# Kernel optimization log

Measured on AMD Instinct MI355X. Metric: run time of the kernel, lower is better.

## Reference

```python
import jax, jax.numpy as jnp
import numpy as np

B, T, D = 4, 4096, 1024
H, HD, K = 16, 64, 32
TAU, THRESHOLD, PULSE_BASE, N_STEPS = 0.1, 0.5, 4.0, 5


def setup_inputs() -> dict:
    key = jax.random.key(0)
    ks = jax.random.split(key, 8)
    s = 0.02
    return {
        "x": jax.random.normal(ks[0], (B, T, D), jnp.float32),
        "spectral_basis": jax.random.normal(ks[1], (B, T, K), jnp.float32) / np.sqrt(T),
        "W_qkv": jax.random.normal(ks[2], (3 * D, D), jnp.float32) * s,
        "W_out": jax.random.normal(ks[3], (D, D), jnp.float32) * s,
        "a": jnp.float32(0.7),
        "b": jnp.float32(0.8),
        "W1": jax.random.normal(ks[4], (HD // 2, HD), jnp.float32) * s,
        "b1": jnp.zeros((HD // 2,), jnp.float32),
        "W2": jax.random.normal(ks[5], (1, HD // 2), jnp.float32) * s,
        "b2": jnp.zeros((1,), jnp.float32),
        "spectral_filter": jnp.full((H, 32), 0.5, jnp.float32),
    }


def soliton_dynamics(stimulus, a, b):
    # stimulus: (B, H, K, HD); FitzHugh-Nagumo style 5-step Euler integration
    dt = 1.0 / N_STEPS
    v = jnp.zeros_like(stimulus)
    w = jnp.zeros_like(stimulus)
    stim_scale = jnp.clip(jnp.max(jnp.abs(stimulus), axis=-1, keepdims=True), 1e-06, None)
    stim_n = stimulus / stim_scale
    I = jnp.where(jnp.abs(stimulus) > THRESHOLD, stim_n, stim_n * 0.1)
    for _ in range(N_STEPS):
        dv = v - v ** 3 / 3 - w + I
        dw = (v + a - b * w) / TAU
        v = jnp.clip(v + dt * dv, -3.0, 3.0)
        w = jnp.clip(w + dt * dw, -3.0, 3.0)
    return v * stim_scale, v


def reference(x, spectral_basis, W_qkv, W_out, a, b, W1, b1, W2, b2, spectral_filter):
    Bx, Tx, Dx = x.shape
    k = spectral_basis.shape[-1]
    qkv = x @ W_qkv.T                                   # (B,T,3D)
    qkv = qkv.reshape(Bx, Tx, 3, H, HD).transpose(2, 0, 3, 1, 4)
    q, kk, v = qkv[0], qkv[1], qkv[2]                   # (B,H,T,HD)

    qm = q.mean(axis=2)                                 # (B,H,HD)
    h1 = jax.nn.silu(qm @ W1.T + b1)
    pulse_widths = PULSE_BASE + jax.nn.softplus(h1 @ W2.T + b2)[..., 0]  # (B,H)

    q_spec = jnp.einsum('bhtd,btk->bhkd', q, spectral_basis)
    k_spec = jnp.einsum('bhtd,btk->bhkd', kk, spectral_basis)
    attn_spec = jnp.einsum('bhkd,bhkd->bhk', q_spec, k_spec) / np.sqrt(HD)
    filt = jax.nn.sigmoid(spectral_filter[:, :k])       # (H,k)
    attn_spec = attn_spec * filt[None]

    stim = jnp.broadcast_to(attn_spec[..., None], (Bx, H, k, HD))
    response, state = soliton_dynamics(stim, a, b)
    response = response.mean(axis=-1)                   # (B,H,k)

    v_spec = jnp.einsum('bhtd,btk->bhkd', v, spectral_basis)
    out_spec = response[..., None] * v_spec             # (B,H,k,HD)
    out = jnp.einsum('bhkd,btk->bhtd', out_spec, spectral_basis)
    out = out.transpose(0, 2, 1, 3).reshape(Bx, Tx, Dx)
    out = out @ W_out.T
    return out, pulse_widths, response
```

## Files before the change

### kernel.cpp

```cpp
#include <hip/hip_runtime.h>

#define B_ 4
#define T_ 4096
#define D_ 1024
#define H_ 16
#define K_ 32


__device__ __forceinline__ void fma4(float4& a, float s, const float4& v){
  a.x = fmaf(s, v.x, a.x); a.y = fmaf(s, v.y, a.y);
  a.z = fmaf(s, v.z, a.z); a.w = fmaf(s, v.w, a.w);
}

__global__ __launch_bounds__(256) void reduce_g(
    const float4* __restrict__ src, float4* __restrict__ dst,
    const int n4, const int zper, const int stride4)
{
  const int g = blockIdx.y;
  int i = blockIdx.x * 256 + threadIdx.x;
  if (i >= n4) return;
  float s0 = 0.f, s1 = 0.f, s2 = 0.f, s3 = 0.f;
  const float4* p = src + (size_t)g * zper * stride4 + i;
  #pragma unroll 8
  for (int zz = 0; zz < zper; ++zz){
    float4 v = p[(size_t)zz * stride4];
    s0 += v.x; s1 += v.y; s2 += v.z; s3 += v.w;
  }
  float4 o; o.x = s0; o.y = s1; o.z = s2; o.w = s3;
  dst[(size_t)g * stride4 + i] = o;
}

__global__ __launch_bounds__(256) void reduce_zp(
    const float4* __restrict__ src, float4* __restrict__ dst,
    const int n4, const int z, const int stride4, const int total4)
{
  int i = blockIdx.x * 256 + threadIdx.x;
  if (i >= total4) return;
  if (i >= n4){
    float4 zv; zv.x = 0.f; zv.y = 0.f; zv.z = 0.f; zv.w = 0.f;
    dst[i] = zv; return;
  }
  float s0 = 0.f, s1 = 0.f, s2 = 0.f, s3 = 0.f;
  const float4* p = src + i;
  #pragma unroll 8
  for (int zz = 0; zz < z; ++zz){
    float4 v = p[(size_t)zz * stride4];
    s0 += v.x; s1 += v.y; s2 += v.z; s3 += v.w;
  }
  float4 o; o.x = s0; o.y = s1; o.z = s2; o.w = s3;
  dst[i] = o;
}

__global__ __launch_bounds__(256) void reduce_z(
    const float4* __restrict__ src, float4* __restrict__ dst,
    const int n4, const int z, const int stride4)
{
  int i = blockIdx.x * 256 + threadIdx.x;
  if (i >= n4) return;
  float s0 = 0.f, s1 = 0.f, s2 = 0.f, s3 = 0.f;
  const float4* p = src + i;
  #pragma unroll 8
  for (int zz = 0; zz < z; ++zz){
    float4 v = p[(size_t)zz * stride4];
    s0 += v.x; s1 += v.y; s2 += v.z; s3 += v.w;
  }
  float4 o; o.x = s0; o.y = s1; o.z = s2; o.w = s3;
  dst[i] = o;
}

__global__ __launch_bounds__(256) void k1_spectral_p(
    const float* __restrict__ x, const float* __restrict__ sb,
    float* __restrict__ XP)
{
  const int ct = blockIdx.x;
  const int b  = blockIdx.y;
  const int zz = blockIdx.z;
  const int t0 = zz * 64;
  const int cs = threadIdx.x & 63;
  const int kg = threadIdx.x >> 6;
  __shared__ __align__(16) float4 xt[4096];
  __shared__ __align__(16) float sbs[64][36];
  #pragma unroll
  for (int i = 0; i < 8; i++){
    int idx = threadIdx.x + i * 256;
    int t = idx >> 5, kk = idx & 31;
    sbs[t][kk] = sb[(size_t)(b * T_ + t0 + t) * K_ + kk];
  }
  const float4* xg = (const float4*)(x + (size_t)(b * T_ + t0) * D_ + ct * 256);
  float4 rv[16];
  #pragma unroll
  for (int j = 0; j < 16; j++){
    int idx = threadIdx.x + j * 256;
    int t = idx >> 6, cq = idx & 63;
    rv[j] = xg[(size_t)t * 256 + cq];
  }
  #pragma unroll
  for (int j = 0; j < 16; j++) xt[threadIdx.x + j * 256] = rv[j];
  __syncthreads();

  float4 acc[8];
  #pragma unroll
  for (int k = 0; k < 8; k++){ acc[k].x = 0.f; acc[k].y = 0.f;
                               acc[k].z = 0.f; acc[k].w = 0.f; }
  float4 am; am.x = 0.f; am.y = 0.f; am.z = 0.f; am.w = 0.f;
  #pragma unroll 4
  for (int t = 0; t < 64; ++t){
    float4 xv = xt[t * 64 + cs];
    if (kg == 0){ am.x += xv.x; am.y += xv.y; am.z += xv.z; am.w += xv.w; }
    const float4* srow = (const float4*)&sbs[t][kg * 8];
    float4 s0 = srow[0], s1 = srow[1];
    fma4(acc[0], s0.x, xv); fma4(acc[1], s0.y, xv);
    fma4(acc[2], s0.z, xv); fma4(acc[3], s0.w, xv);
    fma4(acc[4], s1.x, xv); fma4(acc[5], s1.y, xv);
    fma4(acc[6], s1.z, xv); fma4(acc[7], s1.w, xv);
  }
  const int c = ct * 256 + cs * 4;
  float* o = XP + (size_t)zz * 135168 + (size_t)(b * K_ + kg * 8) * D_ + c;
  #pragma unroll
  for (int k = 0; k < 8; k++) *(float4*)(o + (size_t)k * D_) = acc[k];
  if (kg == 0)
    *(float4*)(XP + (size_t)zz * 135168 + 131072 + b * D_ + c) = am;
}

__global__ __launch_bounds__(256) void gemm_aw_p(
    const float* __restrict__ A, const float* __restrict__ W,
    float* __restrict__ Cp, const int N, const int cPerSplit, const int MN)
{
  __shared__ __align__(16) float As[32][68];
  __shared__ __align__(16) float Ws[32][68];
  const int nt = blockIdx.x, mt = blockIdx.y;
  const int cbase = blockIdx.z * cPerSplit;
  const int tx = threadIdx.x & 15, ty = threadIdx.x >> 4;
  const int sc = threadIdx.x & 31, sr = threadIdx.x >> 5;
  float acc[4][4];
  #pragma unroll
  for (int i = 0; i < 4; i++)
    #pragma unroll
    for (int j = 0; j < 4; j++) acc[i][j] = 0.f;

  float ra[8], rw[8];
  const float* Ap = A + (size_t)(mt * 64 + sr) * 1024 + cbase + sc;
  const float* Wp = W + (size_t)(nt * 64 + sr) * 1024 + cbase + sc;
  #pragma unroll
  for (int i = 0; i < 8; i++){ ra[i] = Ap[(size_t)(i * 8) * 1024];
                               rw[i] = Wp[(size_t)(i * 8) * 1024]; }
  #pragma unroll
  for (int i = 0; i < 8; i++){ As[sc][sr + i * 8] = ra[i];
                               Ws[sc][sr + i * 8] = rw[i]; }
  __syncthreads();

  for (int cc = 32; cc < cPerSplit; cc += 32){
    #pragma unroll
    for (int i = 0; i < 8; i++){ ra[i] = Ap[(size_t)(i * 8) * 1024 + cc];
                                 rw[i] = Wp[(size_t)(i * 8) * 1024 + cc]; }
    #pragma unroll 4
    for (int c = 0; c < 32; ++c){
      const float4 a4 = *(const float4*)&As[c][ty * 4];
      const float4 w4 = *(const float4*)&Ws[c][tx * 4];
      acc[0][0] = fmaf(a4.x, w4.x, acc[0][0]);
      acc[0][1] = fmaf(a4.x, w4.y, acc[0][1]);
      acc[0][2] = fmaf(a4.x, w4.z, acc[0][2]);
      acc[0][3] = fmaf(a4.x, w4.w, acc[0][3]);
      acc[1][0] = fmaf(a4.y, w4.x, acc[1][0]);
      acc[1][1] = fmaf(a4.y, w4.y, acc[1][1]);
      acc[1][2] = fmaf(a4.y, w4.z, acc[1][2]);
      acc[1][3] = fmaf(a4.y, w4.w, acc[1][3]);
      acc[2][0] = fmaf(a4.z, w4.x, acc[2][0]);
      acc[2][1] = fmaf(a4.z, w4.y, acc[2][1]);
      acc[2][2] = fmaf(a4.z, w4.z, acc[2][2]);
      acc[2][3] = fmaf(a4.z, w4.w, acc[2][3]);
      acc[3][0] = fmaf(a4.w, w4.x, acc[3][0]);
      acc[3][1] = fmaf(a4.w, w4.y, acc[3][1]);
      acc[3][2] = fmaf(a4.w, w4.z, acc[3][2]);
      acc[3][3] = fmaf(a4.w, w4.w, acc[3][3]);
    }
    __syncthreads();
    #pragma unroll
    for (int i = 0; i < 8; i++){ As[sc][sr + i * 8] = ra[i];
                                 Ws[sc][sr + i * 8] = rw[i]; }
    __syncthreads();
  }
  #pragma unroll 4
  for (int c = 0; c < 32; ++c){
    const float4 a4 = *(const float4*)&As[c][ty * 4];
    const float4 w4 = *(const float4*)&Ws[c][tx * 4];
    acc[0][0] = fmaf(a4.x, w4.x, acc[0][0]);
    acc[0][1] = fmaf(a4.x, w4.y, acc[0][1]);
    acc[0][2] = fmaf(a4.x, w4.z, acc[0][2]);
    acc[0][3] = fmaf(a4.x, w4.w, acc[0][3]);
    acc[1][0] = fmaf(a4.y, w4.x, acc[1][0]);
    acc[1][1] = fmaf(a4.y, w4.y, acc[1][1]);
    acc[1][2] = fmaf(a4.y, w4.z, acc[1][2]);
    acc[1][3] = fmaf(a4.y, w4.w, acc[1][3]);
    acc[2][0] = fmaf(a4.z, w4.x, acc[2][0]);
    acc[2][1] = fmaf(a4.z, w4.y, acc[2][1]);
    acc[2][2] = fmaf(a4.z, w4.z, acc[2][2]);
    acc[2][3] = fmaf(a4.z, w4.w, acc[2][3]);
    acc[3][0] = fmaf(a4.w, w4.x, acc[3][0]);
    acc[3][1] = fmaf(a4.w, w4.y, acc[3][1]);
    acc[3][2] = fmaf(a4.w, w4.z, acc[3][2]);
    acc[3][3] = fmaf(a4.w, w4.w, acc[3][3]);
  }
  float* cp = Cp + (size_t)blockIdx.z * MN;
  #pragma unroll
  for (int i = 0; i < 4; i++){
    float4 o; o.x = acc[i][0]; o.y = acc[i][1]; o.z = acc[i][2]; o.w = acc[i][3];
    *(float4*)(cp + (size_t)(mt * 64 + ty * 4 + i) * N + nt * 64 + tx * 4) = o;
  }
}

__global__ __launch_bounds__(64) void k3_small(
    const float* __restrict__ qkvC,
    const float* __restrict__ W1, const float* __restrict__ b1,
    const float* __restrict__ W2, const float* __restrict__ b2,
    const float* __restrict__ filt,
    const float* __restrict__ a_in, const float* __restrict__ b_in,
    float* __restrict__ u, float* __restrict__ out_pulse,
    float* __restrict__ out_resp)
{
  const int b = blockIdx.x >> 4, h = blockIdx.x & 15;
  const int d = threadIdx.x;
  __shared__ float qm[64];
  __shared__ float h1s[32];
  __shared__ float rsp[32];
  qm[d] = qkvC[(size_t)(128 + b) * 3072 + h * 64 + d] * (1.0f / 4096.0f);
  __syncthreads();
  if (d < 32){
    float z = b1[d];
    for (int j = 0; j < 64; j++) z = fmaf(qm[j], W1[d * 64 + j], z);
    h1s[d] = z / (1.0f + __expf(-z));
  }
  __syncthreads();
  if (d == 0){
    float z2 = b2[0];
    for (int j = 0; j < 32; j++) z2 = fmaf(h1s[j], W2[j], z2);
    out_pulse[b * H_ + h] = 4.0f + log1pf(__expf(z2));
  }
  if (d < 32){
    const int k = d;
    const float* qrow = qkvC + (size_t)(b * K_ + k) * 3072 + h * 64;
    const float* krow = qrow + 1024;
    float s = 0.f;
    for (int j = 0; j < 64; j++) s = fmaf(qrow[j], krow[j], s);
    float fg = 1.0f / (1.0f + __expf(-filt[h * 32 + k]));
    s = s * 0.125f * fg;
    float av = a_in[0], bv = b_in[0];
    float sc = fmaxf(fabsf(s), 1e-6f);
    float sn = s / sc;
    float I  = (fabsf(s) > 0.5f) ? sn : 0.1f * sn;
    float v = 0.f, w = 0.f;
    #pragma unroll
    for (int it = 0; it < 5; ++it){
      float dv = v - v * v * v * (1.0f / 3.0f) - w + I;
      float dw = (v + av - bv * w) * 10.0f;
      v = fminf(fmaxf(v + 0.2f * dv, -3.0f), 3.0f);
      w = fminf(fmaxf(w + 0.2f * dw, -3.0f), 3.0f);
    }
    float r = v * sc;
    rsp[k] = r;
    out_resp[(b * H_ + h) * K_ + k] = r;
  }
  __syncthreads();
  for (int k = 0; k < 32; k++){
    u[(size_t)(b * K_ + k) * D_ + h * 64 + d] =
        rsp[k] * qkvC[(size_t)(b * K_ + k) * 3072 + 2048 + h * 64 + d];
  }
}

__global__ __launch_bounds__(256) void k4_main(
    const float* __restrict__ sb, const float* __restrict__ Mf,
    float* __restrict__ out)
{
  const int yy = blockIdx.x;
  const int r0 = (yy < 56 ? yy : yy + 8) * 16;
  const int b  = r0 >> 12;
  const int e0 = threadIdx.x * 4;
  __shared__ __align__(16) float sbs[16][36];
  #pragma unroll
  for (int i = 0; i < 2; i++){
    int idx = threadIdx.x + i * 256;
    int k = idx & 31, t = idx >> 5;
    sbs[t][k] = sb[(size_t)(r0 + t) * K_ + k];
  }
  __syncthreads();
  float4 m4[32];
  const float* mp = Mf + (size_t)b * K_ * D_ + e0;
  #pragma unroll
  for (int k = 0; k < 32; k++) m4[k] = *(const float4*)(mp + (size_t)k * D_);
  float* op = out + (size_t)r0 * D_ + e0;
  #pragma unroll 4
  for (int t = 0; t < 16; ++t){
    float4 o4; o4.x = 0.f; o4.y = 0.f; o4.z = 0.f; o4.w = 0.f;
    const float4* srow = (const float4*)&sbs[t][0];
    #pragma unroll
    for (int j = 0; j < 8; j++){
      float4 s4 = srow[j];
      fma4(o4, s4.x, m4[j * 4 + 0]);
      fma4(o4, s4.y, m4[j * 4 + 1]);
      fma4(o4, s4.z, m4[j * 4 + 2]);
      fma4(o4, s4.w, m4[j * 4 + 3]);
    }
    *(float4*)(op + (size_t)t * D_) = o4;
  }
}

__global__ __launch_bounds__(256) void k4_tailp(
    const float* __restrict__ sb, const float* __restrict__ Mf,
    float* __restrict__ out)
{
  __shared__ float sbs[128][33];
  __shared__ __align__(16) float Ms[32][16];
  const int j = blockIdx.x;
  #pragma unroll
  for (int i = 0; i < 2; i++){
    int idx = threadIdx.x + i * 256;
    int k = idx >> 4, e = idx & 15;
    Ms[k][e] = Mf[(size_t)k * D_ + j * 16 + e];
  }
  #pragma unroll
  for (int i = 0; i < 16; i++){
    int idx = threadIdx.x + i * 256;
    int k = idx & 31, t = idx >> 5;
    sbs[t][k] = sb[(size_t)(896 + t) * K_ + k];
  }
  __syncthreads();
  const int t  = threadIdx.x >> 1;
  const int c0 = (threadIdx.x & 1) * 8;
  float a0 = 0.f, a1 = 0.f, a2 = 0.f, a3 = 0.f;
  float a4 = 0.f, a5 = 0.f, a6 = 0.f, a7 = 0.f;
  #pragma unroll
  for (int k = 0; k < 32; k++){
    float s = sbs[t][k];
    const float4 m0 = *(const float4*)&Ms[k][c0];
    const float4 m1 = *(const float4*)&Ms[k][c0 + 4];
    a0 = fmaf(s, m0.x, a0); a1 = fmaf(s, m0.y, a1);
    a2 = fmaf(s, m0.z, a2); a3 = fmaf(s, m0.w, a3);
    a4 = fmaf(s, m1.x, a4); a5 = fmaf(s, m1.y, a5);
    a6 = fmaf(s, m1.z, a6); a7 = fmaf(s, m1.w, a7);
  }
  float* op = out + (size_t)(896 + t) * D_ + j * 16 + c0;
  float4 o0; o0.x = a0; o0.y = a1; o0.z = a2; o0.w = a3;
  float4 o1; o1.x = a4; o1.y = a5; o1.z = a6; o1.w = a7;
  *(float4*)(op)     = o0;
  *(float4*)(op + 4) = o1;
}

extern "C" void kernel_launch(void* const* d_in, const int* in_sizes, int n_in,
                              void* d_out, int out_size, void* d_ws, size_t ws_size,
                              hipStream_t stream)
{
  const float* x    = (const float*)d_in[0];
  const float* sb   = (const float*)d_in[1];
  const float* Wqkv = (const float*)d_in[2];
  const float* Wout = (const float*)d_in[3];
  const float* a_in = (const float*)d_in[4];
  const float* b_in = (const float*)d_in[5];
  const float* W1   = (const float*)d_in[6];
  const float* b1   = (const float*)d_in[7];
  const float* W2   = (const float*)d_in[8];
  const float* b2   = (const float*)d_in[9];
  const float* filt = (const float*)d_in[10];

  float* outF = (float*)d_out;
  float* qkv  = outF + 196608;
  float* u    = outF + 786432;
  float* Mm   = outF + 917504;
  float* S    = outF + 1048576;
  float* S2   = outF + 9699328;
  float* S3   = outF + 5242880;
  float* pulse = outF + 16777216;
  float* resp  = outF + 16777280;

  k1_spectral_p<<<dim3(4, 4, 64), 256, 0, stream>>>(x, sb, S);
  reduce_g<<<dim3(132, 8), 256, 0, stream>>>((const float4*)S, (float4*)S2,
                                             33792, 8, 33792);
  reduce_zp<<<dim3(192), 256, 0, stream>>>((const float4*)S2, (float4*)outF,
                                           33792, 8, 33792, 49152);

  gemm_aw_p<<<dim3(48, 3, 16), 256, 0, stream>>>(outF, Wqkv, S, 3072, 64, 589824);
  reduce_z<<<dim3(576), 256, 0, stream>>>((const float4*)S, (float4*)qkv,
                                          147456, 16, 147456);

  k3_small<<<dim3(64), dim3(64), 0, stream>>>(qkv, W1, b1, W2, b2,
                                              filt, a_in, b_in, u,
                                              pulse, resp);

  gemm_aw_p<<<dim3(16, 2, 32), 256, 0, stream>>>(u, Wout, S, 1024, 32, 131072);
  reduce_g<<<dim3(128, 8), 256, 0, stream>>>((const float4*)S, (float4*)S3,
                                             32768, 4, 32768);
  reduce_z<<<dim3(128), 256, 0, stream>>>((const float4*)S3, (float4*)Mm,
                                          32768, 8, 32768);

  k4_main<<<dim3(1016), 256, 0, stream>>>(sb, Mm, outF);
  k4_tailp<<<dim3(64), 256, 0, stream>>>(sb, Mm, outF);
}
```

Before: 261.2 us.

## Retile k4_main: each thread computes 8 rows x 4 columns, streaming M rows

Restructures the final basis-expansion kernel. Each block now covers 32 time rows and 256 output columns, and each thread accumulates 8 rows by 4 columns while streaming M rows from global memory. Previously each thread held 32 float4 M values in registers across 16 rows. The spectral basis tile is stored transposed in shared memory so a thread can read its 8 row coefficients as two float4 loads. This aims to cut register pressure and raise occupancy and reuse, at the cost of reading M more often, with those reads going through cache.

```diff
diff --git a/kernel.cpp b/kernel.cpp
--- a/kernel.cpp
+++ b/kernel.cpp
@@ -271,37 +271,40 @@
     const float* __restrict__ sb, const float* __restrict__ Mf,
     float* __restrict__ out)
 {
-  const int yy = blockIdx.x;
-  const int r0 = (yy < 56 ? yy : yy + 8) * 16;
+  const int ct = blockIdx.x;
+  const int yy = blockIdx.y;
+  const int r0 = (yy < 28 ? yy : yy + 4) * 32;
   const int b  = r0 >> 12;
-  const int e0 = threadIdx.x * 4;
-  __shared__ __align__(16) float sbs[16][36];
-  #pragma unroll
-  for (int i = 0; i < 2; i++){
+  const int w  = threadIdx.x >> 6;
+  const int ls = threadIdx.x & 63;
+  __shared__ __align__(16) float sbsT[32][36];
+  #pragma unroll
+  for (int i = 0; i < 4; i++){
     int idx = threadIdx.x + i * 256;
-    int k = idx & 31, t = idx >> 5;
-    sbs[t][k] = sb[(size_t)(r0 + t) * K_ + k];
-  }
-  __syncthreads();
-  float4 m4[32];
-  const float* mp = Mf + (size_t)b * K_ * D_ + e0;
-  #pragma unroll
-  for (int k = 0; k < 32; k++) m4[k] = *(const float4*)(mp + (size_t)k * D_);
-  float* op = out + (size_t)r0 * D_ + e0;
-  #pragma unroll 4
-  for (int t = 0; t < 16; ++t){
-    float4 o4; o4.x = 0.f; o4.y = 0.f; o4.z = 0.f; o4.w = 0.f;
-    const float4* srow = (const float4*)&sbs[t][0];
-    #pragma unroll
-    for (int j = 0; j < 8; j++){
-      float4 s4 = srow[j];
-      fma4(o4, s4.x, m4[j * 4 + 0]);
-      fma4(o4, s4.y, m4[j * 4 + 1]);
-      fma4(o4, s4.z, m4[j * 4 + 2]);
-      fma4(o4, s4.w, m4[j * 4 + 3]);
-    }
-    *(float4*)(op + (size_t)t * D_) = o4;
-  }
+    int t = idx >> 5, k = idx & 31;
+    sbsT[k][t] = sb[(size_t)(r0 + t) * K_ + k];
+  }
+  __syncthreads();
+  float4 acc[8];
+  #pragma unroll
+  for (int i = 0; i < 8; i++){ acc[i].x = 0.f; acc[i].y = 0.f;
+                               acc[i].z = 0.f; acc[i].w = 0.f; }
+  const float4* Mg = (const float4*)(Mf + (size_t)b * K_ * D_);
+  const int eq = ct * 64 + ls;
+  #pragma unroll 8
+  for (int k = 0; k < 32; ++k){
+    float4 mv = Mg[(size_t)k * 256 + eq];
+    const float4* srow = (const float4*)&sbsT[k][w * 8];
+    float4 s0 = srow[0], s1 = srow[1];
+    fma4(acc[0], s0.x, mv); fma4(acc[1], s0.y, mv);
+    fma4(acc[2], s0.z, mv); fma4(acc[3], s0.w, mv);
+    fma4(acc[4], s1.x, mv); fma4(acc[5], s1.y, mv);
+    fma4(acc[6], s1.z, mv); fma4(acc[7], s1.w, mv);
+  }
+  float* op = out + (size_t)(r0 + w * 8) * D_ + eq * 4;
+  #pragma unroll
+  for (int i = 0; i < 8; i++)
+    *(float4*)(op + (size_t)i * D_) = acc[i];
 }
 
 __global__ __launch_bounds__(256) void k4_tailp(
@@ -391,6 +394,6 @@
   reduce_z<<<dim3(128), 256, 0, stream>>>((const float4*)S3, (float4*)Mm,
                                           32768, 8, 32768);
 
-  k4_main<<<dim3(1016), 256, 0, stream>>>(sb, Mm, outF);
+  k4_main<<<dim3(4, 508), 256, 0, stream>>>(sb, Mm, outF);
   k4_tailp<<<dim3(64), 256, 0, stream>>>(sb, Mm, outF);
 }
```

Measured after the change: 238.4 us. 8.7% less time.
